# Optimization experiments

Hardware: AMD Instinct MI355X
Metric: run time of the kernel (lower is better)

## Reference

```python
import jax, jax.numpy as jnp
import numpy as np

H = 16
D_MODEL = 1024
D_K = D_MODEL // H
B = 4
S = 2048
NEG = -1000000000.0


def setup_inputs() -> dict:
    key = jax.random.key(0)
    ks = jax.random.split(key, 12)
    def lin(k):
        # torch nn.Linear default init: U(-1/sqrt(fan_in), 1/sqrt(fan_in))
        bound = 1.0 / np.sqrt(D_MODEL)
        kw, kb = jax.random.split(k)
        W = jax.random.uniform(kw, (D_MODEL, D_MODEL), jnp.float32, -bound, bound)
        b = jax.random.uniform(kb, (D_MODEL,), jnp.float32, -bound, bound)
        return W, b
    Wq, bq = lin(ks[0]); Wk, bk = lin(ks[1]); Wv, bv = lin(ks[2]); Wo, bo = lin(ks[3])
    return {
        "query": jax.random.normal(ks[4], (B, S, D_MODEL), jnp.float32),
        "key": jax.random.normal(ks[5], (B, S, D_MODEL), jnp.float32),
        "value": jax.random.normal(ks[6], (B, S, D_MODEL), jnp.float32),
        "mask": jax.random.randint(ks[7], (B, S, S), 0, 2, jnp.int32),
        "Wq": Wq, "bq": bq, "Wk": Wk, "bk": bk,
        "Wv": Wv, "bv": bv, "Wo": Wo, "bo": bo,
    }


def reference(query, key, value, mask, Wq, bq, Wk, bk, Wv, bv, Wo, bo):
    # project and split heads: [B,S,D] -> [B,H,S,Dk]
    def proj(x, W, b):
        y = x @ W.T + b
        return y.reshape(B, S, H, D_K).transpose(0, 2, 1, 3)
    q = proj(query, Wq, bq)
    k = proj(key, Wk, bk)
    v = proj(value, Wv, bv)
    m = mask[:, None, :, :]  # [B,1,S,S]
    scores = jnp.einsum("bhqd,bhkd->bhqk", q, k) / jnp.sqrt(jnp.float32(D_K))
    scores = jnp.where(m == 0, NEG, scores)
    p_attn = jax.nn.softmax(scores, axis=-1)
    p_attn = jnp.where(m == 0, 0.0, p_attn)  # faithful to second masked_fill
    x = jnp.einsum("bhqk,bhkd->bhqd", p_attn, v)
    x = x.transpose(0, 2, 1, 3).reshape(B, S, D_MODEL)
    return x @ Wo.T + bo
```

## Files before the change

kernel.cpp:

```cpp
#include <hip/hip_runtime.h>

typedef __attribute__((ext_vector_type(8))) short short8;
typedef __attribute__((ext_vector_type(4))) float f32x4;

#define B_ 4
#define S_ 2048
#define H_ 16
#define DM 1024
#define DK 64

#define QSCALE 0.18033688011112042f

__device__ __forceinline__ unsigned short f2b(float f) {
  unsigned int u = __float_as_uint(f);
  u += 0x7fff + ((u >> 16) & 1);
  return (unsigned short)(u >> 16);
}

__device__ __forceinline__ void gload_lds16(const void* g, void* l) {
  __builtin_amdgcn_global_load_lds(
      (const __attribute__((address_space(1))) unsigned int*)g,
      (__attribute__((address_space(3))) unsigned int*)l, 16, 0, 0);
}

__global__ __launch_bounds__(256) void cvt_kernel(
    const float* __restrict__ a0, const float* __restrict__ a1,
    const float* __restrict__ a2, const float* __restrict__ a3,
    unsigned short* __restrict__ out, int n_per) {
  const float* src = (blockIdx.z == 0) ? a0 : (blockIdx.z == 1) ? a1
                   : (blockIdx.z == 2) ? a2 : a3;
  unsigned short* dst = out + (size_t)blockIdx.z * n_per;
  int i = (blockIdx.x * 256 + threadIdx.x) * 8;
  if (i >= n_per) return;
  float4 x0 = *(const float4*)&src[i];
  float4 x1 = *(const float4*)&src[i + 4];
  alignas(16) unsigned short r[8] = {f2b(x0.x), f2b(x0.y), f2b(x0.z), f2b(x0.w),
                                     f2b(x1.x), f2b(x1.y), f2b(x1.z), f2b(x1.w)};
  *(uint4*)&dst[i] = *(const uint4*)r;
}

__global__ __launch_bounds__(256) void pack_kernel(const int* __restrict__ m,
                                                   unsigned int* __restrict__ out) {
  size_t i = (size_t)blockIdx.x * 256 + threadIdx.x;
  unsigned long long w = __ballot(m[i] != 0);
  if ((threadIdx.x & 31) == 0)
    out[i >> 5] = (unsigned int)(w >> (threadIdx.x & 32));
}

__device__ __forceinline__ void gemm128(
    const unsigned short* __restrict__ A, const unsigned short* __restrict__ W,
    const float* __restrict__ bias, float scale, int mode,
    unsigned short* __restrict__ outb, float* __restrict__ outf) {
  __shared__ unsigned short Sh[128 * 132];
  unsigned short* As = Sh;
  unsigned short* Bs = Sh + 128 * 64;
  const int m0 = blockIdx.x * 128;
  const int n0 = blockIdx.y * 128;
  const int t = threadIdx.x;
  const int lane = t & 63, wave = t >> 6;
  const int lr = lane & 15, quad = lane >> 4;
  const int wm = (wave >> 1) * 64, wn = (wave & 1) * 64;
  const int srow = (lane >> 3);
  const int scol = ((lane & 7) ^ srow) * 8;
  const int cs0 = (quad ^ (lr & 7)) * 8;
  const int cs1 = ((4 + quad) ^ (lr & 7)) * 8;

  const f32x4 zv = {0.f, 0.f, 0.f, 0.f};
  f32x4 acc[4][4];
#pragma unroll
  for (int mt = 0; mt < 4; mt++)
#pragma unroll
    for (int nt = 0; nt < 4; nt++) acc[mt][nt] = zv;

  for (int kb = 0; kb < DM; kb += 64) {
    __syncthreads();
#pragma unroll
    for (int i = 0; i < 4; i++) {
      int c = wave * 4 + i;
      int row = c * 8 + srow;
      gload_lds16(&A[(size_t)(m0 + row) * DM + kb + scol], &As[c * 512]);
      gload_lds16(&W[(size_t)(n0 + row) * DM + kb + scol], &Bs[c * 512]);
    }
    __syncthreads();
#pragma unroll
    for (int ks = 0; ks < 2; ks++) {
      const int cc = ks ? cs1 : cs0;
      short8 af[4], bf[4];
#pragma unroll
      for (int mt = 0; mt < 4; mt++)
        af[mt] = *(const short8*)&As[(wm + mt * 16 + lr) * 64 + cc];
#pragma unroll
      for (int nt = 0; nt < 4; nt++)
        bf[nt] = *(const short8*)&Bs[(wn + nt * 16 + lr) * 64 + cc];
#pragma unroll
      for (int mt = 0; mt < 4; mt++)
#pragma unroll
        for (int nt = 0; nt < 4; nt++)
          acc[mt][nt] = __builtin_amdgcn_mfma_f32_16x16x32_bf16(af[mt], bf[nt], acc[mt][nt], 0, 0, 0);
    }
  }

  if (mode == 1) {
    __syncthreads();
#pragma unroll
    for (int mt = 0; mt < 4; mt++) {
#pragma unroll
      for (int nt = 0; nt < 4; nt++) {
        int n = wn + nt * 16 + lr;
        int m = wm + mt * 16 + quad * 4;
        float bn = bias[n0 + n];
        alignas(8) unsigned short p4[4];
#pragma unroll
        for (int reg = 0; reg < 4; reg++)
          p4[reg] = f2b((acc[mt][nt][reg] + bn) * scale);
        *(uint2*)&Sh[n * 132 + m] = *(const uint2*)p4;
      }
    }
    __syncthreads();
    int n = t >> 1, mh = (t & 1) * 64;
    int gn = n0 + n;
    int h = gn >> 6, dk = gn & 63;
    int b = m0 >> 11, s0 = (m0 & (S_ - 1)) + mh;
    size_t obase = (size_t)((b * H_ + h) * 64 + dk) * S_ + s0;
#pragma unroll
    for (int c = 0; c < 8; c++)
      *(uint4*)&outb[obase + c * 8] = *(const uint4*)&Sh[n * 132 + mh + c * 8];
    return;
  }

#pragma unroll
  for (int mt = 0; mt < 4; mt++) {
#pragma unroll
    for (int nt = 0; nt < 4; nt++) {
#pragma unroll
      for (int reg = 0; reg < 4; reg++) {
        int gm = m0 + wm + mt * 16 + quad * 4 + reg;
        int gn = n0 + wn + nt * 16 + lr;
        float v = (acc[mt][nt][reg] + bias[gn]) * scale;
        if (mode == 0) {
          int b = gm >> 11, s = gm & (S_ - 1);
          int h = gn >> 6, dk = gn & 63;
          outb[(((size_t)(b * H_ + h) * S_ + s) << 6) + dk] = f2b(v);
        } else {
          outf[(size_t)gm * DM + gn] = v;
        }
      }
    }
  }
}

__global__ __launch_bounds__(256) void gemm_qkv_kernel(
    const unsigned short* __restrict__ xb, const unsigned short* __restrict__ wb,
    const float* __restrict__ bq, const float* __restrict__ bk, const float* __restrict__ bv,
    unsigned short* __restrict__ q_out, unsigned short* __restrict__ k_out,
    unsigned short* __restrict__ v_out) {
  int z = blockIdx.z;
  const unsigned short* A = xb + (size_t)z * (B_ * S_ * DM);
  const unsigned short* W = wb + (size_t)z * (DM * DM);
  const float* bias = (z == 0) ? bq : (z == 1) ? bk : bv;
  unsigned short* ob = (z == 0) ? q_out : (z == 1) ? k_out : v_out;
  gemm128(A, W, bias, (z == 0) ? QSCALE : 1.0f, (z == 2) ? 1 : 0, ob, nullptr);
}

__global__ __launch_bounds__(256) void gemm_out_kernel(
    const unsigned short* __restrict__ ab, const unsigned short* __restrict__ wb,
    const float* __restrict__ bo, float* __restrict__ out) {
  gemm128(ab, wb + (size_t)3 * (DM * DM), bo, 1.0f, 2, nullptr, out);
}

__global__ __launch_bounds__(256, 3) void attn_kernel(
    const unsigned short* __restrict__ qb, const unsigned short* __restrict__ kb,
    const unsigned short* __restrict__ vt, const unsigned int* __restrict__ mbits,
    unsigned short* __restrict__ ao) {
  __shared__ unsigned short Ks[2][64 * 64];
  __shared__ unsigned short Vs[2][64 * 64];
  __shared__ unsigned short Pl[4][32 * 72];
  const int bh = blockIdx.x;
  const int b = bh >> 4, h = bh & 15;
  const int t = threadIdx.x, lane = t & 63, wave = t >> 6;
  const int lr = lane & 15, quad = lane >> 4;
  const int q0 = blockIdx.y * 128 + wave * 32;
  const unsigned short* qp = qb + (size_t)bh * S_ * DK;
  const unsigned short* kp = kb + (size_t)bh * S_ * DK;
  const unsigned short* vp = vt + (size_t)bh * DK * S_;
  const unsigned int* mrow = mbits + (size_t)b * S_ * (S_ / 32);
  unsigned short* plw = &Pl[wave][0];

  const int trow = t >> 3;
  const int tsw = ((t & 7) ^ (trow & 7)) * 8;
  const int wbase = wave * 512;
  const int c0 = (quad ^ (lr & 7)) * 8;
  const int c1 = ((4 + quad) ^ (lr & 7)) * 8;
  const unsigned int sh0 = 31 - lr, sh1 = 15 - lr;

  short8 qf[2][2];
#pragma unroll
  for (int mt = 0; mt < 2; mt++)
#pragma unroll
    for (int ks = 0; ks < 2; ks++)
      qf[mt][ks] = *(const short8*)&qp[(size_t)(q0 + mt * 16 + lr) * DK + ks * 32 + quad * 8];

  const f32x4 zv = {0.f, 0.f, 0.f, 0.f};
  short8 ones;
#pragma unroll
  for (int i = 0; i < 8; i++) ones[i] = (short)0x3F80;
  f32x4 oacc[2][4], lacc[2];
#pragma unroll
  for (int mt = 0; mt < 2; mt++) {
    lacc[mt] = zv;
#pragma unroll
    for (int nt = 0; nt < 4; nt++) oacc[mt][nt] = zv;
  }

#define STAGE(KT, BUF) do {                                                   \
    int kb2 = (KT) * 64;                                                      \
    gload_lds16(kp + (size_t)(kb2 + trow) * DK + tsw,      &Ks[BUF][wbase]);  \
    gload_lds16(kp + (size_t)(kb2 + 32 + trow) * DK + tsw, &Ks[BUF][2048 + wbase]); \
    gload_lds16(vp + (size_t)trow * S_ + kb2 + tsw,        &Vs[BUF][wbase]);  \
    gload_lds16(vp + (size_t)(32 + trow) * S_ + kb2 + tsw, &Vs[BUF][2048 + wbase]); \
  } while (0)

  auto body = [&](int kt, int buf) {
    uint2 mw[2][4];
#pragma unroll
    for (int mt = 0; mt < 2; mt++)
#pragma unroll
      for (int r = 0; r < 4; r++)
        mw[mt][r] = *(const uint2*)&mrow[(size_t)(q0 + mt * 16 + quad * 4 + r) * (S_ / 32) + kt * 2];

    f32x4 sacc[2][4];
#pragma unroll
    for (int nt = 0; nt < 4; nt++) {
      short8 kf0 = *(const short8*)&Ks[buf][(nt * 16 + lr) * 64 + c0];
      short8 kf1 = *(const short8*)&Ks[buf][(nt * 16 + lr) * 64 + c1];
#pragma unroll
      for (int mt = 0; mt < 2; mt++) {
        f32x4 z = __builtin_amdgcn_mfma_f32_16x16x32_bf16(qf[mt][0], kf0, zv, 0, 0, 0);
        sacc[mt][nt] = __builtin_amdgcn_mfma_f32_16x16x32_bf16(qf[mt][1], kf1, z, 0, 0, 0);
      }
    }
#pragma unroll
    for (int mt = 0; mt < 2; mt++) {
#pragma unroll
      for (int r = 0; r < 4; r++) {
        uint2 m2 = mw[mt][r];
#pragma unroll
        for (int nt = 0; nt < 4; nt++) {
          unsigned int w = (nt < 2) ? m2.x : m2.y;
          unsigned int shl = (nt & 1) ? sh1 : sh0;
          float e = exp2f(sacc[mt][nt][r]);
          unsigned int pb = (__float_as_uint(e) + 0x8000u) >> 16;
          pb &= (unsigned int)(((int)(w << shl)) >> 31);
          plw[(mt * 16 + quad * 4 + r) * 72 + nt * 16 + lr] = (unsigned short)pb;
        }
      }
    }
    short8 pf[2][2];
#pragma unroll
    for (int mt = 0; mt < 2; mt++)
#pragma unroll
      for (int ks = 0; ks < 2; ks++)
        pf[mt][ks] = *(const short8*)&plw[(mt * 16 + lr) * 72 + ks * 32 + quad * 8];
#pragma unroll
    for (int mt = 0; mt < 2; mt++) {
      lacc[mt] = __builtin_amdgcn_mfma_f32_16x16x32_bf16(pf[mt][0], ones, lacc[mt], 0, 0, 0);
      lacc[mt] = __builtin_amdgcn_mfma_f32_16x16x32_bf16(pf[mt][1], ones, lacc[mt], 0, 0, 0);
    }
#pragma unroll
    for (int nt = 0; nt < 4; nt++) {
      short8 vf0 = *(const short8*)&Vs[buf][(nt * 16 + lr) * 64 + c0];
      short8 vf1 = *(const short8*)&Vs[buf][(nt * 16 + lr) * 64 + c1];
#pragma unroll
      for (int mt = 0; mt < 2; mt++) {
        oacc[mt][nt] = __builtin_amdgcn_mfma_f32_16x16x32_bf16(pf[mt][0], vf0, oacc[mt][nt], 0, 0, 0);
        oacc[mt][nt] = __builtin_amdgcn_mfma_f32_16x16x32_bf16(pf[mt][1], vf1, oacc[mt][nt], 0, 0, 0);
      }
    }
  };

  STAGE(0, 0);
  for (int kt = 0; kt < S_ / 64; kt += 2) {
    __syncthreads();
    STAGE(kt + 1, 1);
    body(kt, 0);
    __syncthreads();
    if (kt + 2 < S_ / 64) STAGE(kt + 2, 0);
    body(kt + 1, 1);
  }
#undef STAGE

#pragma unroll
  for (int mt = 0; mt < 2; mt++) {
#pragma unroll
    for (int r = 0; r < 4; r++) {
      float l = lacc[mt][r];
      float inv = (l > 0.f) ? 1.f / l : 0.f;
      int row = q0 + mt * 16 + quad * 4 + r;
#pragma unroll
      for (int nt = 0; nt < 4; nt++)
        ao[((size_t)(b * S_ + row) * DM) + h * 64 + nt * 16 + lr] =
            f2b(oacc[mt][nt][r] * inv);
    }
  }
}

extern "C" void kernel_launch(void* const* d_in, const int* in_sizes, int n_in,
                              void* d_out, int out_size, void* d_ws, size_t ws_size,
                              hipStream_t stream) {
  const float* query = (const float*)d_in[0];
  const float* key   = (const float*)d_in[1];
  const float* value = (const float*)d_in[2];
  const int*   mask  = (const int*)d_in[3];
  const float* Wq = (const float*)d_in[4];
  const float* bq = (const float*)d_in[5];
  const float* Wk = (const float*)d_in[6];
  const float* bk = (const float*)d_in[7];
  const float* Wv = (const float*)d_in[8];
  const float* bv = (const float*)d_in[9];
  const float* Wo = (const float*)d_in[10];
  const float* bo = (const float*)d_in[11];
  float* out = (float*)d_out;
  char* ws = (char*)d_ws;

  unsigned short* qb = (unsigned short*)(ws);
  unsigned short* kbf = (unsigned short*)(ws + 16777216);
  unsigned short* vt = (unsigned short*)(ws + 33554432);
  unsigned short* wb = (unsigned short*)(ws + 50331648);
  unsigned int*   mb = (unsigned int*)(ws + 58720256);
  unsigned short* xb = (unsigned short*)(ws + 60817408);
  unsigned short* ao = (unsigned short*)(ws + 60817408);

  cvt_kernel<<<dim3(4096, 1, 3), 256, 0, stream>>>(query, key, value, nullptr, xb, B_ * S_ * DM);
  cvt_kernel<<<dim3(512, 1, 4), 256, 0, stream>>>(Wq, Wk, Wv, Wo, wb, DM * DM);
  pack_kernel<<<dim3(65536), 256, 0, stream>>>(mask, mb);
  gemm_qkv_kernel<<<dim3(64, 8, 3), 256, 0, stream>>>(xb, wb, bq, bk, bv, qb, kbf, vt);
  attn_kernel<<<dim3(64, 16), 256, 0, stream>>>(qb, kbf, vt, mb, ao);
  gemm_out_kernel<<<dim3(64, 8), 256, 0, stream>>>(ao, wb, bo, out);
}
```

Measured before the change: 444.0 us.

## Keep attention probabilities in registers via transposed QK and permlane swaps

```diff
diff --git a/kernel.cpp b/kernel.cpp
--- a/kernel.cpp
+++ b/kernel.cpp
@@ -15,6 +15,12 @@
   unsigned int u = __float_as_uint(f);
   u += 0x7fff + ((u >> 16) & 1);
   return (unsigned short)(u >> 16);
+}
+
+__device__ __forceinline__ unsigned int cvtpk_bf16(float lo, float hi) {
+  unsigned int r;
+  asm("v_cvt_pk_bf16_f32 %0, %1, %2" : "=v"(r) : "v"(lo), "v"(hi));
+  return r;
 }
 
 __device__ __forceinline__ void gload_lds16(const void* g, void* l) {
@@ -168,13 +174,12 @@
   gemm128(ab, wb + (size_t)3 * (DM * DM), bo, 1.0f, 2, nullptr, out);
 }
 
-__global__ __launch_bounds__(256, 3) void attn_kernel(
+__global__ __launch_bounds__(256, 4) void attn_kernel(
     const unsigned short* __restrict__ qb, const unsigned short* __restrict__ kb,
     const unsigned short* __restrict__ vt, const unsigned int* __restrict__ mbits,
     unsigned short* __restrict__ ao) {
   __shared__ unsigned short Ks[2][64 * 64];
   __shared__ unsigned short Vs[2][64 * 64];
-  __shared__ unsigned short Pl[4][32 * 72];
   const int bh = blockIdx.x;
   const int b = bh >> 4, h = bh & 15;
   const int t = threadIdx.x, lane = t & 63, wave = t >> 6;
@@ -184,14 +189,17 @@
   const unsigned short* kp = kb + (size_t)bh * S_ * DK;
   const unsigned short* vp = vt + (size_t)bh * DK * S_;
   const unsigned int* mrow = mbits + (size_t)b * S_ * (S_ / 32);
-  unsigned short* plw = &Pl[wave][0];
 
   const int trow = t >> 3;
   const int tsw = ((t & 7) ^ (trow & 7)) * 8;
   const int wbase = wave * 512;
   const int c0 = (quad ^ (lr & 7)) * 8;
   const int c1 = ((4 + quad) ^ (lr & 7)) * 8;
-  const unsigned int sh0 = 31 - lr, sh1 = 15 - lr;
+  const int brev = ((quad & 1) << 1) | (quad >> 1);
+  const int vc0 = (brev ^ (lr & 7)) * 8;
+  const int vc1 = ((4 + brev) ^ (lr & 7)) * 8;
+  const int shA = 28 - quad * 4;
+  const int shB = 12 - quad * 4;
 
   short8 qf[2][2];
 #pragma unroll
@@ -221,59 +229,59 @@
   } while (0)
 
   auto body = [&](int kt, int buf) {
-    uint2 mw[2][4];
+    uint2 mq[2];
 #pragma unroll
     for (int mt = 0; mt < 2; mt++)
-#pragma unroll
-      for (int r = 0; r < 4; r++)
-        mw[mt][r] = *(const uint2*)&mrow[(size_t)(q0 + mt * 16 + quad * 4 + r) * (S_ / 32) + kt * 2];
-
-    f32x4 sacc[2][4];
-#pragma unroll
-    for (int nt = 0; nt < 4; nt++) {
-      short8 kf0 = *(const short8*)&Ks[buf][(nt * 16 + lr) * 64 + c0];
-      short8 kf1 = *(const short8*)&Ks[buf][(nt * 16 + lr) * 64 + c1];
+      mq[mt] = *(const uint2*)&mrow[(size_t)(q0 + mt * 16 + lr) * (S_ / 32) + kt * 2];
+
+#pragma unroll
+    for (int ks = 0; ks < 2; ks++) {
+      f32x4 sc[2][2];
+#pragma unroll
+      for (int ntl = 0; ntl < 2; ntl++) {
+        int nt = 2 * ks + ntl;
+        short8 kf0 = *(const short8*)&Ks[buf][(nt * 16 + lr) * 64 + c0];
+        short8 kf1 = *(const short8*)&Ks[buf][(nt * 16 + lr) * 64 + c1];
+#pragma unroll
+        for (int mt = 0; mt < 2; mt++) {
+          f32x4 z = __builtin_amdgcn_mfma_f32_16x16x32_bf16(kf0, qf[mt][0], zv, 0, 0, 0);
+          sc[mt][ntl] = __builtin_amdgcn_mfma_f32_16x16x32_bf16(kf1, qf[mt][1], z, 0, 0, 0);
+        }
+      }
+      short8 pf[2];
 #pragma unroll
       for (int mt = 0; mt < 2; mt++) {
-        f32x4 z = __builtin_amdgcn_mfma_f32_16x16x32_bf16(qf[mt][0], kf0, zv, 0, 0, 0);
-        sacc[mt][nt] = __builtin_amdgcn_mfma_f32_16x16x32_bf16(qf[mt][1], kf1, z, 0, 0, 0);
-      }
-    }
-#pragma unroll
-    for (int mt = 0; mt < 2; mt++) {
-#pragma unroll
-      for (int r = 0; r < 4; r++) {
-        uint2 m2 = mw[mt][r];
-#pragma unroll
-        for (int nt = 0; nt < 4; nt++) {
-          unsigned int w = (nt < 2) ? m2.x : m2.y;
-          unsigned int shl = (nt & 1) ? sh1 : sh0;
-          float e = exp2f(sacc[mt][nt][r]);
-          unsigned int pb = (__float_as_uint(e) + 0x8000u) >> 16;
-          pb &= (unsigned int)(((int)(w << shl)) >> 31);
-          plw[(mt * 16 + quad * 4 + r) * 72 + nt * 16 + lr] = (unsigned short)pb;
+        unsigned int w = ks ? mq[mt].y : mq[mt].x;
+        unsigned int tA = w << shA;
+        unsigned int tB = w << shB;
+        float pa[4], pb[4];
+#pragma unroll
+        for (int r = 0; r < 4; r++) {
+          unsigned int sxA = (unsigned int)((int)(tA << (3 - r)) >> 31);
+          unsigned int sxB = (unsigned int)((int)(tB << (3 - r)) >> 31);
+          pa[r] = __uint_as_float(__float_as_uint(exp2f(sc[mt][0][r])) & sxA);
+          pb[r] = __uint_as_float(__float_as_uint(exp2f(sc[mt][1][r])) & sxB);
         }
-      }
-    }
-    short8 pf[2][2];
-#pragma unroll
-    for (int mt = 0; mt < 2; mt++)
-#pragma unroll
-      for (int ks = 0; ks < 2; ks++)
-        pf[mt][ks] = *(const short8*)&plw[(mt * 16 + lr) * 72 + ks * 32 + quad * 8];
-#pragma unroll
-    for (int mt = 0; mt < 2; mt++) {
-      lacc[mt] = __builtin_amdgcn_mfma_f32_16x16x32_bf16(pf[mt][0], ones, lacc[mt], 0, 0, 0);
-      lacc[mt] = __builtin_amdgcn_mfma_f32_16x16x32_bf16(pf[mt][1], ones, lacc[mt], 0, 0, 0);
-    }
-#pragma unroll
-    for (int nt = 0; nt < 4; nt++) {
-      short8 vf0 = *(const short8*)&Vs[buf][(nt * 16 + lr) * 64 + c0];
-      short8 vf1 = *(const short8*)&Vs[buf][(nt * 16 + lr) * 64 + c1];
-#pragma unroll
-      for (int mt = 0; mt < 2; mt++) {
-        oacc[mt][nt] = __builtin_amdgcn_mfma_f32_16x16x32_bf16(pf[mt][0], vf0, oacc[mt][nt], 0, 0, 0);
-        oacc[mt][nt] = __builtin_amdgcn_mfma_f32_16x16x32_bf16(pf[mt][1], vf1, oacc[mt][nt], 0, 0, 0);
+        unsigned int A0 = cvtpk_bf16(pa[0], pa[1]);
+        unsigned int A1 = cvtpk_bf16(pa[2], pa[3]);
+        unsigned int B0 = cvtpk_bf16(pb[0], pb[1]);
+        unsigned int B1 = cvtpk_bf16(pb[2], pb[3]);
+        asm("v_permlane16_swap_b32 %0, %1" : "+v"(A0), "+v"(B0));
+        asm("v_permlane16_swap_b32 %0, %1" : "+v"(A1), "+v"(B1));
+        union { unsigned int u[4]; short8 s8; } un;
+        un.u[0] = A0; un.u[1] = A1; un.u[2] = B0; un.u[3] = B1;
+        pf[mt] = un.s8;
+      }
+#pragma unroll
+      for (int mt = 0; mt < 2; mt++)
+        lacc[mt] = __builtin_amdgcn_mfma_f32_16x16x32_bf16(pf[mt], ones, lacc[mt], 0, 0, 0);
+      const int vc = ks ? vc1 : vc0;
+#pragma unroll
+      for (int nt = 0; nt < 4; nt++) {
+        short8 vf = *(const short8*)&Vs[buf][(nt * 16 + lr) * 64 + vc];
+#pragma unroll
+        for (int mt = 0; mt < 2; mt++)
+          oacc[mt][nt] = __builtin_amdgcn_mfma_f32_16x16x32_bf16(pf[mt], vf, oacc[mt][nt], 0, 0, 0);
       }
     }
   };
```

New measurement: 428.2 us. -3.6%, faster.
